# Kernel optimization log

Measured on AMD Instinct MI355X. Metric: run time of the kernel, lower is better.

Reference implementation:

```python
import jax, jax.numpy as jnp
import numpy as np
from jax import lax

BN_EPS = 1e-5


def setup_inputs() -> dict:
    key = jax.random.key(0)
    ks = jax.random.split(key, 8)
    B, C, H, W = 2, 256, 64, 64
    Cr = C // 4
    return {
        "x": jax.random.normal(ks[0], (B, C, H, W), jnp.float32),
        "conv_w": jax.random.normal(ks[1], (Cr, C, 3, 3), jnp.float32) * 0.02,
        "conv_b": jax.random.normal(ks[2], (Cr,), jnp.float32) * 0.02,
        "bn_gamma": jax.random.uniform(ks[3], (Cr,), jnp.float32, 0.5, 1.5),
        "bn_beta": jax.random.normal(ks[4], (Cr,), jnp.float32) * 0.1,
        "bn_mean": jax.random.normal(ks[5], (Cr,), jnp.float32) * 0.1,
        "bn_var": jax.random.uniform(ks[6], (Cr,), jnp.float32, 0.5, 1.5),
        "prelu_w": jnp.full((1,), 0.25, jnp.float32),
    }


def reference(x, conv_w, conv_b, bn_gamma, bn_beta, bn_mean, bn_var, prelu_w):
    B, C, H, W = x.shape
    N = H * W
    # conv_match: 3x3 conv (pad=1) -> BatchNorm (inference) -> PReLU
    y = lax.conv_general_dilated(
        x, conv_w, window_strides=(1, 1), padding="SAME",
        dimension_numbers=("NCHW", "OIHW", "NCHW"))
    y = y + conv_b[None, :, None, None]
    scale = bn_gamma / jnp.sqrt(bn_var + BN_EPS)
    y = (y - bn_mean[None, :, None, None]) * scale[None, :, None, None] + bn_beta[None, :, None, None]
    y = jnp.where(y >= 0, y, prelu_w[0] * y)  # PReLU, single shared slope

    e = y.reshape(B, -1, N)                       # [B, Cr, N]
    sim = jnp.einsum("bdn,bdm->bnm", e, e)        # [B, N, N]
    sim = sim - jnp.max(sim, axis=2, keepdims=True)

    # sparsemax along last dim
    srt = -jnp.sort(-sim, axis=2)                 # descending sort
    cs = jnp.cumsum(srt, axis=2) - 1.0
    ar = jnp.arange(1, N + 1, dtype=sim.dtype)[None, None, :]
    mask = ar * srt > cs
    k = jnp.sum(mask, axis=2, keepdims=True)      # int support size, [B,N,1]
    tau = jnp.take_along_axis(cs, k - 1, axis=2) / k.astype(sim.dtype)
    p = jnp.maximum(sim - tau, 0.0)               # sparsemax probs [B,N,N]

    out = jnp.einsum("bcn,bnm->bcm", x.reshape(B, C, N), p)
    return out.reshape(B, C, H, W) + x
```

## Files before the change

kernel.cpp:

```cpp
#include <hip/hip_runtime.h>
#include <math.h>

#define NPIX 4096
#define CR   64
#define CIN  256
#define HW   64
#define CSPLIT 8

typedef __attribute__((ext_vector_type(8))) short s16x8;
typedef __attribute__((ext_vector_type(4))) float f32x4;

__device__ __forceinline__ unsigned short f2bf(float f) {
  union { float f; unsigned u; } a; a.f = f;
  return (unsigned short)((a.u + 0x7FFF + ((a.u >> 16) & 1)) >> 16);
}
__device__ __forceinline__ float bf2f(unsigned short h) {
  union { unsigned u; float f; } a; a.u = (unsigned)h << 16; return a.f;
}

__global__ __launch_bounds__(256) void k_conv_part(
    const float* __restrict__ x, const float* __restrict__ cw,
    float* __restrict__ pp) {
  const int hg = blockIdx.x;
  const int dg = blockIdx.y;
  const int b  = blockIdx.z >> 3;
  const int cs = blockIdx.z & 7;
  const int h0 = hg * 2, d0 = dg * 32, c0 = cs * 32;
  const int tid = threadIdx.x;
  const int wp = tid & 31;
  const int dq = tid >> 5;
  const int w0 = wp * 2;

  __shared__ float xs[16][4][68];
  __shared__ float wl[16][9][32];

  float acc[2][2][4] = {};

  for (int cc = 0; cc < 32; cc += 16) {
    __syncthreads();
    for (int i = tid; i < 16 * 256; i += 256) {
      int c = i >> 8, r = (i >> 6) & 3, w = i & 63;
      int row = h0 - 1 + r;
      float v = 0.f;
      if (row >= 0 && row < HW)
        v = x[((size_t)(b * CIN + c0 + cc + c) << 12) + row * HW + w];
      xs[c][r][w + 1] = v;
    }
    if (tid < 128) {
      int c = tid >> 3, r = (tid >> 1) & 3, s = tid & 1;
      xs[c][r][s ? 65 : 0] = 0.f;
    }
    for (int i = tid; i < 16 * 9 * 32; i += 256) {
      int c = i / 288, rem = i - c * 288, tap = rem >> 5, d = rem & 31;
      wl[c][tap][d] = cw[(size_t)(d0 + d) * 2304 + (c0 + cc + c) * 9 + tap];
    }
    __syncthreads();

#pragma unroll 2
    for (int c = 0; c < 16; ++c) {
      float xv[4][4];
#pragma unroll
      for (int r = 0; r < 4; ++r) {
        float2 p0 = *(const float2*)&xs[c][r][w0];
        float2 p1 = *(const float2*)&xs[c][r][w0 + 2];
        xv[r][0] = p0.x; xv[r][1] = p0.y; xv[r][2] = p1.x; xv[r][3] = p1.y;
      }
#pragma unroll
      for (int tap = 0; tap < 9; ++tap) {
        const int kh = tap / 3, kw = tap - kh * 3;
        float4 wv = *(const float4*)&wl[c][tap][dq * 4];
        float wf[4] = {wv.x, wv.y, wv.z, wv.w};
#pragma unroll
        for (int hi = 0; hi < 2; ++hi)
#pragma unroll
          for (int wi = 0; wi < 2; ++wi) {
            float xvv = xv[hi + kh][wi + kw];
#pragma unroll
            for (int di = 0; di < 4; ++di)
              acc[hi][wi][di] = fmaf(wf[di], xvv, acc[hi][wi][di]);
          }
      }
    }
  }
#pragma unroll
  for (int di = 0; di < 4; ++di) {
    int d = d0 + dq * 4 + di;
#pragma unroll
    for (int hi = 0; hi < 2; ++hi)
#pragma unroll
      for (int wi = 0; wi < 2; ++wi)
        pp[((size_t)((b * CSPLIT + cs) * 64 + d) << 12) + (h0 + hi) * HW + w0 + wi] =
            acc[hi][wi][di];
  }
}

__global__ __launch_bounds__(256) void k_bn(
    const float* __restrict__ pp, const float* __restrict__ cb,
    const float* __restrict__ gamma, const float* __restrict__ beta,
    const float* __restrict__ mean, const float* __restrict__ var,
    const float* __restrict__ pw, unsigned short* __restrict__ eTh,
    unsigned short* __restrict__ eTl) {
  const int n0 = blockIdx.x * 64;
  const int b  = blockIdx.y;
  const int tid = threadIdx.x;
  __shared__ float et[64][65];

  const float slope = pw[0];
#pragma unroll 4
  for (int dd = 0; dd < 16; ++dd) {
    int d = dd * 4 + (tid >> 6);
    int n = tid & 63;
    float s = 0.f;
#pragma unroll
    for (int cs = 0; cs < CSPLIT; ++cs)
      s += pp[((size_t)((b * CSPLIT + cs) * 64 + d) << 12) + n0 + n];
    float scale = gamma[d] / sqrtf(var[d] + 1e-5f);
    float y = (s + cb[d] - mean[d]) * scale + beta[d];
    y = (y >= 0.f) ? y : slope * y;
    et[d][n] = y;
  }
  __syncthreads();
#pragma unroll 4
  for (int w = 0; w < 16; ++w) {
    int n = w * 4 + (tid >> 6);
    int d = tid & 63;
    float v = et[d][n];
    unsigned short hi = f2bf(v);
    unsigned short lo = f2bf(v - bf2f(hi));
    size_t off = (((size_t)b << 12) + n0 + n) * 64 + d;
    eTh[off] = hi;
    eTl[off] = lo;
  }
}

__global__ __launch_bounds__(1024) void k_gsm(
    const unsigned short* __restrict__ eTh, const unsigned short* __restrict__ eTl,
    unsigned short* __restrict__ p, unsigned char* __restrict__ flags) {
  const int n0 = blockIdx.x * 16;
  const int b  = blockIdx.y;
  const int tid = threadIdx.x;
  const int l = tid & 63, wid = tid >> 6;
  const int lc = l & 15, lq = l >> 4;

  __shared__ __align__(16) unsigned short eah[16][72];
  __shared__ __align__(16) unsigned short eal[16][72];
  __shared__ float rs[16][16];
  __shared__ int   rc[16][16];
  __shared__ float stau[16];
  __shared__ int   sprev[16];
  __shared__ int   schg;

  const size_t ebase = ((size_t)b << 12) * 64;

  {
    int d = tid & 63, r = (tid >> 6) & 15;
    size_t off = ebase + (size_t)(n0 + r) * 64 + d;
    eah[r][d] = eTh[off];
    eal[r][d] = eTl[off];
  }
  if (tid < 16) sprev[tid] = NPIX + 1;
  __syncthreads();

  f32x4 acc[16];
#pragma unroll
  for (int t = 0; t < 16; ++t)
#pragma unroll
    for (int q = 0; q < 4; ++q) acc[t][q] = 0.f;

  const int mbase = wid * 256;
#pragma unroll
  for (int kc = 0; kc < 2; ++kc) {
    s16x8 ah = *(const s16x8*)&eah[lc][kc * 32 + lq * 8];
    s16x8 al = *(const s16x8*)&eal[lc][kc * 32 + lq * 8];
#pragma unroll
    for (int t = 0; t < 16; ++t) {
      size_t off = ebase + (size_t)(mbase + t * 16 + lc) * 64 + kc * 32 + lq * 8;
      s16x8 bh = *(const s16x8*)&eTh[off];
      s16x8 bl = *(const s16x8*)&eTl[off];
      acc[t] = __builtin_amdgcn_mfma_f32_16x16x32_bf16(ah, bh, acc[t], 0, 0, 0);
      acc[t] = __builtin_amdgcn_mfma_f32_16x16x32_bf16(ah, bl, acc[t], 0, 0, 0);
      acc[t] = __builtin_amdgcn_mfma_f32_16x16x32_bf16(al, bh, acc[t], 0, 0, 0);
    }
  }

  {
    float mx[4];
#pragma unroll
    for (int q = 0; q < 4; ++q) {
      float m = acc[0][q];
#pragma unroll
      for (int t = 1; t < 16; ++t) m = fmaxf(m, acc[t][q]);
      mx[q] = m;
    }
#pragma unroll
    for (int o = 1; o <= 8; o <<= 1)
#pragma unroll
      for (int q = 0; q < 4; ++q) mx[q] = fmaxf(mx[q], __shfl_xor(mx[q], o));
    if (lc == 0)
#pragma unroll
      for (int q = 0; q < 4; ++q) rs[wid][lq * 4 + q] = mx[q];
  }
  __syncthreads();
  if (tid < 16) {
    float m = rs[0][tid];
#pragma unroll
    for (int w = 1; w < 16; ++w) m = fmaxf(m, rs[w][tid]);
    stau[tid] = m - 1.0f;
  }

  for (int it = 0; it < 64; ++it) {
    __syncthreads();
    float tl[4];
#pragma unroll
    for (int q = 0; q < 4; ++q) tl[q] = stau[lq * 4 + q];
    if (tid == 0) schg = 0;
    float s[4]; int c[4];
#pragma unroll
    for (int q = 0; q < 4; ++q) { s[q] = 0.f; c[q] = 0; }
#pragma unroll
    for (int t = 0; t < 16; ++t)
#pragma unroll
      for (int q = 0; q < 4; ++q) {
        float v = acc[t][q];
        if (v > tl[q]) { s[q] += v; ++c[q]; }
      }
#pragma unroll
    for (int o = 1; o <= 8; o <<= 1)
#pragma unroll
      for (int q = 0; q < 4; ++q) {
        s[q] += __shfl_xor(s[q], o);
        c[q] += __shfl_xor(c[q], o);
      }
    if (lc == 0)
#pragma unroll
      for (int q = 0; q < 4; ++q) { rs[wid][lq * 4 + q] = s[q]; rc[wid][lq * 4 + q] = c[q]; }
    __syncthreads();
    if (tid < 16) {
      float ss = 0.f; int cc = 0;
#pragma unroll
      for (int w = 0; w < 16; ++w) { ss += rs[w][tid]; cc += rc[w][tid]; }
      stau[tid] = (ss - 1.f) / (float)cc;
      if (cc != sprev[tid]) { sprev[tid] = cc; schg = 1; }
    }
    __syncthreads();
    if (schg == 0) break;
  }

  float tw[4];
#pragma unroll
  for (int q = 0; q < 4; ++q) tw[q] = stau[lq * 4 + q];
  int any0 = 0, any1 = 0;
#pragma unroll
  for (int t = 0; t < 16; ++t) {
#pragma unroll
    for (int q = 0; q < 4; ++q) {
      float pv = fmaxf(acc[t][q] - tw[q], 0.f);
      if (t < 8) any0 |= (pv > 0.f); else any1 |= (pv > 0.f);
      p[((size_t)(b * NPIX + n0 + lq * 4 + q) << 12) + mbase + t * 16 + lc] =
          f2bf(pv);
    }
  }
  unsigned long long b0 = __ballot(any0), b1 = __ballot(any1);
  if (l == 0) {
    int kt = n0 >> 5;
    if (b0) flags[(b << 12) | ((wid * 2 + 0) << 7) | kt] = 1;
    if (b1) flags[(b << 12) | ((wid * 2 + 1) << 7) | kt] = 1;
  }
}

__global__ __launch_bounds__(256) void k_out_mfma(
    const unsigned short* __restrict__ pb, const float* __restrict__ x,
    float* __restrict__ out, const unsigned char* __restrict__ flags) {
  const int m0 = blockIdx.x * 128;
  const int c0 = blockIdx.y * 64;
  const int b  = blockIdx.z;
  const int tid = threadIdx.x;
  const int l = tid & 63, wid = tid >> 6;
  const int wr = wid >> 1, wc = wid & 1;

  __shared__ unsigned short As[64][42];
  __shared__ unsigned short Bs[128][42];
  __shared__ unsigned char fl[128];

  if (tid < 128)
    fl[tid] = flags[((size_t)b << 12) | ((size_t)blockIdx.x << 7) | (size_t)tid];

  f32x4 acc[2][4];
#pragma unroll
  for (int i = 0; i < 2; ++i)
#pragma unroll
    for (int j = 0; j < 4; ++j)
#pragma unroll
      for (int q = 0; q < 4; ++q) acc[i][j][q] = 0.f;

  const int arow = tid >> 2;
  const int akc  = (tid & 3) * 8;
  const float* axsrc = x + ((size_t)(b * CIN + c0 + arow) << 12) + akc;
  const int bm = (tid & 31) * 4;
  const int bk = (tid >> 5) * 4;
  const unsigned short* bsrc = pb + ((size_t)(b * NPIX + bk) << 12) + m0 + bm;

  __syncthreads();

  for (int k0 = 0; k0 < NPIX; k0 += 32) {
    if (!fl[k0 >> 5]) continue;
    __syncthreads();
    float4 A0 = *(const float4*)(axsrc + k0);
    float4 A1 = *(const float4*)(axsrc + k0 + 4);
    s16x8 ap;
    ap[0] = (short)f2bf(A0.x); ap[1] = (short)f2bf(A0.y);
    ap[2] = (short)f2bf(A0.z); ap[3] = (short)f2bf(A0.w);
    ap[4] = (short)f2bf(A1.x); ap[5] = (short)f2bf(A1.y);
    ap[6] = (short)f2bf(A1.z); ap[7] = (short)f2bf(A1.w);
    *(s16x8*)&As[arow][akc] = ap;
    const unsigned short* bp = bsrc + ((size_t)k0 << 12);
    ushort4 L0 = *(const ushort4*)(bp);
    ushort4 L1 = *(const ushort4*)(bp + 4096);
    ushort4 L2 = *(const ushort4*)(bp + 8192);
    ushort4 L3 = *(const ushort4*)(bp + 12288);
    *(ushort4*)&Bs[bm + 0][bk] = make_ushort4(L0.x, L1.x, L2.x, L3.x);
    *(ushort4*)&Bs[bm + 1][bk] = make_ushort4(L0.y, L1.y, L2.y, L3.y);
    *(ushort4*)&Bs[bm + 2][bk] = make_ushort4(L0.z, L1.z, L2.z, L3.z);
    *(ushort4*)&Bs[bm + 3][bk] = make_ushort4(L0.w, L1.w, L2.w, L3.w);
    __syncthreads();

    s16x8 a[2], bb[4];
    const int kg = l >> 4;
#pragma unroll
    for (int i = 0; i < 2; ++i) {
      int row = wr * 32 + i * 16 + (l & 15);
      a[i] = *(const s16x8*)&As[row][kg * 8];
    }
#pragma unroll
    for (int j = 0; j < 4; ++j) {
      int n = wc * 64 + j * 16 + (l & 15);
      bb[j] = *(const s16x8*)&Bs[n][kg * 8];
    }
#pragma unroll
    for (int i = 0; i < 2; ++i)
#pragma unroll
      for (int j = 0; j < 4; ++j)
        acc[i][j] = __builtin_amdgcn_mfma_f32_16x16x32_bf16(
            a[i], bb[j], acc[i][j], 0, 0, 0);
  }

#pragma unroll
  for (int i = 0; i < 2; ++i)
#pragma unroll
    for (int j = 0; j < 4; ++j)
#pragma unroll
      for (int q = 0; q < 4; ++q) {
        int c = c0 + wr * 32 + i * 16 + (l >> 4) * 4 + q;
        int m = m0 + wc * 64 + j * 16 + (l & 15);
        size_t off = ((size_t)(b * CIN + c) << 12) + m;
        out[off] = acc[i][j][q] + x[off];
      }
}

extern "C" void kernel_launch(void* const* d_in, const int* in_sizes, int n_in,
                              void* d_out, int out_size, void* d_ws, size_t ws_size,
                              hipStream_t stream) {
  const float* x     = (const float*)d_in[0];
  const float* cw    = (const float*)d_in[1];
  const float* cb    = (const float*)d_in[2];
  const float* gamma = (const float*)d_in[3];
  const float* beta  = (const float*)d_in[4];
  const float* mean  = (const float*)d_in[5];
  const float* var   = (const float*)d_in[6];
  const float* pw    = (const float*)d_in[7];
  float* out = (float*)d_out;

  unsigned short* p_bf = (unsigned short*)d_ws;
  float* pp  = (float*)((char*)d_ws + ((size_t)64 << 20));
  unsigned short* eTh = (unsigned short*)((char*)d_ws + ((size_t)80 << 20));
  unsigned short* eTl = (unsigned short*)((char*)d_ws + ((size_t)81 << 20));
  unsigned char* flags = (unsigned char*)((char*)d_ws + ((size_t)84 << 20));

  hipMemsetAsync(flags, 0, 2 * 32 * 128, stream);
  k_conv_part<<<dim3(32, 2, 16), 256, 0, stream>>>(x, cw, pp);
  k_bn<<<dim3(64, 2), 256, 0, stream>>>(pp, cb, gamma, beta, mean, var, pw,
                                        eTh, eTl);
  k_gsm<<<dim3(NPIX / 16, 2), 1024, 0, stream>>>(eTh, eTl, p_bf, flags);
  k_out_mfma<<<dim3(32, 4, 2), 256, 0, stream>>>(p_bf, x, out, flags);
}
```

Measured before the change: 295.0 us.

## Permute pixel order in embeddings for vectorized P stores and finer skip flags

Within each group of 256 pixels, pixel indices are stored permuted so that each sparsemax block processes a strided set of rows. This lets every lane write 16 contiguous bf16 outputs as two 128-bit stores instead of scattered 2-byte stores. Skip flags now cover 16-row stripes instead of 32-row tiles, and the output GEMM zero-fills the B tile for an empty half instead of loading it. The risk is that rows which were contiguous are now spread out, which could make the skip flags sparser or denser and depends on how the sparsemax support is distributed.

Result: faster. 287.1 us (-2.7%).

```diff
diff --git a/kernel.cpp b/kernel.cpp
--- a/kernel.cpp
+++ b/kernel.cpp
@@ -127,7 +127,10 @@
     float v = et[d][n];
     unsigned short hi = f2bf(v);
     unsigned short lo = f2bf(v - bf2f(hi));
-    size_t off = (((size_t)b << 12) + n0 + n) * 64 + d;
+    int nl = n0 + n;
+    int g = nl >> 8, i = nl & 255;
+    int np = (g << 8) | ((i & 15) << 4) | (i >> 4);
+    size_t off = (((size_t)b << 12) + np) * 64 + d;
     eTh[off] = hi;
     eTl[off] = lo;
   }
@@ -154,7 +157,9 @@
 
   {
     int d = tid & 63, r = (tid >> 6) & 15;
-    size_t off = ebase + (size_t)(n0 + r) * 64 + d;
+    int g = n0 >> 8, a = (n0 & 255) >> 4;
+    int np = (g << 8) | (r << 4) | a;
+    size_t off = ebase + (size_t)np * 64 + d;
     eah[r][d] = eTh[off];
     eal[r][d] = eTl[off];
   }
@@ -249,22 +254,41 @@
   float tw[4];
 #pragma unroll
   for (int q = 0; q < 4; ++q) tw[q] = stau[lq * 4 + q];
-  int any0 = 0, any1 = 0;
-#pragma unroll
-  for (int t = 0; t < 16; ++t) {
+  s16x8 oA[4], oB[4];
+  int anyL = 0;
+#pragma unroll
+  for (int q = 0; q < 4; ++q) {
+#pragma unroll
+    for (int t = 0; t < 8; ++t) {
+      float pv = fmaxf(acc[t][q] - tw[q], 0.f);
+      anyL |= (pv > 0.f);
+      oA[q][t] = (short)f2bf(pv);
+    }
+#pragma unroll
+    for (int t = 0; t < 8; ++t) {
+      float pv = fmaxf(acc[t + 8][q] - tw[q], 0.f);
+      anyL |= (pv > 0.f);
+      oB[q][t] = (short)f2bf(pv);
+    }
+  }
+  unsigned long long bal = __ballot(anyL != 0);
+  const unsigned long long M0 = 0x00FF00FF00FF00FFULL;
+  bool w0 = (bal & M0) != 0;
+  bool w1 = (bal & ~M0) != 0;
+  bool mine = (lc < 8) ? w0 : w1;
+  if (mine) {
 #pragma unroll
     for (int q = 0; q < 4; ++q) {
-      float pv = fmaxf(acc[t][q] - tw[q], 0.f);
-      if (t < 8) any0 |= (pv > 0.f); else any1 |= (pv > 0.f);
-      p[((size_t)(b * NPIX + n0 + lq * 4 + q) << 12) + mbase + t * 16 + lc] =
-          f2bf(pv);
-    }
-  }
-  unsigned long long b0 = __ballot(any0), b1 = __ballot(any1);
+      unsigned short* pr =
+          p + ((size_t)(b * NPIX + n0 + lq * 4 + q) << 12) + mbase + lc * 16;
+      *(s16x8*)pr = oA[q];
+      *(s16x8*)(pr + 8) = oB[q];
+    }
+  }
   if (l == 0) {
-    int kt = n0 >> 5;
-    if (b0) flags[(b << 12) | ((wid * 2 + 0) << 7) | kt] = 1;
-    if (b1) flags[(b << 12) | ((wid * 2 + 1) << 7) | kt] = 1;
+    int stripe = blockIdx.x;
+    if (w0) flags[(b << 13) | ((wid * 2 + 0) << 8) | stripe] = 1;
+    if (w1) flags[(b << 13) | ((wid * 2 + 1) << 8) | stripe] = 1;
   }
 }
 
@@ -280,10 +304,9 @@
 
   __shared__ unsigned short As[64][42];
   __shared__ unsigned short Bs[128][42];
-  __shared__ unsigned char fl[128];
-
-  if (tid < 128)
-    fl[tid] = flags[((size_t)b << 12) | ((size_t)blockIdx.x << 7) | (size_t)tid];
+  __shared__ unsigned char fl[256];
+
+  fl[tid] = flags[(b << 13) | (blockIdx.x << 8) | tid];
 
   f32x4 acc[2][4];
 #pragma unroll
@@ -299,11 +322,14 @@
   const int bm = (tid & 31) * 4;
   const int bk = (tid >> 5) * 4;
   const unsigned short* bsrc = pb + ((size_t)(b * NPIX + bk) << 12) + m0 + bm;
+  const int myhalf = bk >> 4;
 
   __syncthreads();
 
   for (int k0 = 0; k0 < NPIX; k0 += 32) {
-    if (!fl[k0 >> 5]) continue;
+    const int s0 = k0 >> 4;
+    const int have0 = fl[s0], have1 = fl[s0 + 1];
+    if (!have0 && !have1) continue;
     __syncthreads();
     float4 A0 = *(const float4*)(axsrc + k0);
     float4 A1 = *(const float4*)(axsrc + k0 + 4);
@@ -313,15 +339,23 @@
     ap[4] = (short)f2bf(A1.x); ap[5] = (short)f2bf(A1.y);
     ap[6] = (short)f2bf(A1.z); ap[7] = (short)f2bf(A1.w);
     *(s16x8*)&As[arow][akc] = ap;
-    const unsigned short* bp = bsrc + ((size_t)k0 << 12);
-    ushort4 L0 = *(const ushort4*)(bp);
-    ushort4 L1 = *(const ushort4*)(bp + 4096);
-    ushort4 L2 = *(const ushort4*)(bp + 8192);
-    ushort4 L3 = *(const ushort4*)(bp + 12288);
-    *(ushort4*)&Bs[bm + 0][bk] = make_ushort4(L0.x, L1.x, L2.x, L3.x);
-    *(ushort4*)&Bs[bm + 1][bk] = make_ushort4(L0.y, L1.y, L2.y, L3.y);
-    *(ushort4*)&Bs[bm + 2][bk] = make_ushort4(L0.z, L1.z, L2.z, L3.z);
-    *(ushort4*)&Bs[bm + 3][bk] = make_ushort4(L0.w, L1.w, L2.w, L3.w);
+    if ((myhalf ? have1 : have0)) {
+      const unsigned short* bp = bsrc + ((size_t)k0 << 12);
+      ushort4 L0 = *(const ushort4*)(bp);
+      ushort4 L1 = *(const ushort4*)(bp + 4096);
+      ushort4 L2 = *(const ushort4*)(bp + 8192);
+      ushort4 L3 = *(const ushort4*)(bp + 12288);
+      *(ushort4*)&Bs[bm + 0][bk] = make_ushort4(L0.x, L1.x, L2.x, L3.x);
+      *(ushort4*)&Bs[bm + 1][bk] = make_ushort4(L0.y, L1.y, L2.y, L3.y);
+      *(ushort4*)&Bs[bm + 2][bk] = make_ushort4(L0.z, L1.z, L2.z, L3.z);
+      *(ushort4*)&Bs[bm + 3][bk] = make_ushort4(L0.w, L1.w, L2.w, L3.w);
+    } else {
+      ushort4 zz = make_ushort4(0, 0, 0, 0);
+      *(ushort4*)&Bs[bm + 0][bk] = zz;
+      *(ushort4*)&Bs[bm + 1][bk] = zz;
+      *(ushort4*)&Bs[bm + 2][bk] = zz;
+      *(ushort4*)&Bs[bm + 3][bk] = zz;
+    }
     __syncthreads();
 
     s16x8 a[2], bb[4];
@@ -376,7 +410,7 @@
   unsigned short* eTl = (unsigned short*)((char*)d_ws + ((size_t)81 << 20));
   unsigned char* flags = (unsigned char*)((char*)d_ws + ((size_t)84 << 20));
 
-  hipMemsetAsync(flags, 0, 2 * 32 * 128, stream);
+  hipMemsetAsync(flags, 0, 2 * 32 * 256, stream);
   k_conv_part<<<dim3(32, 2, 16), 256, 0, stream>>>(x, cw, pp);
   k_bn<<<dim3(64, 2), 256, 0, stream>>>(pp, cb, gamma, beta, mean, var, pw,
                                         eTh, eTl);
```
